# Kernel optimization log

Hardware: AMD Instinct MI355X
Metric: run time of the kernel (lower is better)

Reference implementation:

```python
import jax, jax.numpy as jnp
import numpy as np


def _sine_theta(v1, v2):
    # v1, v2: [..., 2] edge direction vectors
    cross = v1[..., 0] * v2[..., 1] - v1[..., 1] * v2[..., 0]
    k = jnp.linalg.norm(v1, axis=-1) * jnp.linalg.norm(v2, axis=-1)
    return cross / k


def setup_inputs() -> dict:
    key = jax.random.key(0)
    P, N = 16384, 1024  # P polygons, N points each (N % 4 == 0)
    x_list = jax.random.normal(key, (P, N, 2), dtype=jnp.float32)
    return {"x_list": x_list, "scale": 1}


def reference(x_list, scale):
    # x_list: [P, N, 2] stacked polygons (equivalent to the original python list
    # when all polygons have the same point count N).
    P, N, _ = x_list.shape
    segn = N // 4
    # close the polygon and form consecutive edge vectors v[k] = x[k+1] - x[k]
    xc = jnp.concatenate([x_list, x_list[:, :1]], axis=1)  # [P, N+1, 2]
    v = xc[:, 1:] - xc[:, :-1]                             # [P, N, 2]
    idx = jnp.arange(segn) * 3
    v1 = v[:, idx]       # edge i*3
    v2 = v[:, idx + 1]   # edge i*3+1
    v3 = v[:, idx + 2]   # edge i*3+2
    s12 = _sine_theta(v1, v2)   # [P, segn]
    sina = _sine_theta(v1, v3)  # [P, segn]
    direct = (s12 >= 0).astype(x_list.dtype)
    term = direct * jax.nn.relu(-sina) + (1.0 - direct) * jax.nn.relu(sina)
    seg_loss = term.sum(axis=1) / segn  # [P]
    return (seg_loss * scale).mean()
```

## Files before the change

### kernel.cpp

```cpp
#include <hip/hip_runtime.h>


#define N_PTS     1024
#define SEGN      (N_PTS / 4)
#define BLOCK     256
#define ROW_F4    385

__global__ __launch_bounds__(BLOCK)
void xing_partial_kernel(const float* __restrict__ x,
                         float*       __restrict__ partial)
{
    const int p = blockIdx.x;
    const int t = threadIdx.x;

    __shared__ float rowf[ROW_F4 * 4];

    const float4* src = reinterpret_cast<const float4*>(x + (size_t)p * (N_PTS * 2));
    float4* dst = reinterpret_cast<float4*>(rowf);
    dst[t] = src[t];
    if (t < ROW_F4 - BLOCK) dst[BLOCK + t] = src[BLOCK + t];
    __syncthreads();

    const float2* pts = reinterpret_cast<const float2*>(rowf);
    const float2 a = pts[3 * t + 0];
    const float2 b = pts[3 * t + 1];
    const float2 c = pts[3 * t + 2];
    const float2 d = pts[3 * t + 3];

    const float v1x = b.x - a.x, v1y = b.y - a.y;
    const float v2x = c.x - b.x, v2y = c.y - b.y;
    const float v3x = d.x - c.x, v3y = d.y - c.y;

    const float cross12 = v1x * v2y - v1y * v2x;
    const float cross13 = v1x * v3y - v1y * v3x;

    const float n1 = v1x * v1x + v1y * v1y;
    const float n3 = v3x * v3x + v3y * v3y;
    const float sina = cross13 * rsqrtf(n1 * n3);

    float term = (cross12 >= 0.0f) ? fmaxf(-sina, 0.0f) : fmaxf(sina, 0.0f);

    #pragma unroll
    for (int off = 32; off > 0; off >>= 1)
        term += __shfl_down(term, off, 64);

    __shared__ float wsum[BLOCK / 64];
    const int lane = t & 63;
    const int wid  = t >> 6;
    if (lane == 0) wsum[wid] = term;
    __syncthreads();

    if (t == 0) {
        partial[p] = (wsum[0] + wsum[1]) + (wsum[2] + wsum[3]);
    }
}

__global__ __launch_bounds__(BLOCK)
void xing_reduce_kernel(const float* __restrict__ partial,
                        const int*   __restrict__ scale_p,
                        float*       __restrict__ out,
                        int P)
{
    const int t = threadIdx.x;
    const float4* pf4 = reinterpret_cast<const float4*>(partial);
    const int nf4 = P / 4;

    float sum = 0.0f;
    for (int i = t; i < nf4; i += BLOCK) {
        float4 v = pf4[i];
        sum += (v.x + v.y) + (v.z + v.w);
    }

    #pragma unroll
    for (int off = 32; off > 0; off >>= 1)
        sum += __shfl_down(sum, off, 64);

    __shared__ float wsum[BLOCK / 64];
    const int lane = t & 63;
    const int wid  = t >> 6;
    if (lane == 0) wsum[wid] = sum;
    __syncthreads();

    if (t == 0) {
        const float total = (wsum[0] + wsum[1]) + (wsum[2] + wsum[3]);
        out[0] = total * (float)(*scale_p) / ((float)SEGN * (float)P);
    }
}

extern "C" void kernel_launch(void* const* d_in, const int* in_sizes, int n_in,
                              void* d_out, int out_size, void* d_ws, size_t ws_size,
                              hipStream_t stream)
{
    const float* x       = (const float*)d_in[0];
    const int*   scale_p = (const int*)d_in[1];
    float*       out     = (float*)d_out;
    float*       partial = (float*)d_ws;

    const int P = in_sizes[0] / (N_PTS * 2);

    xing_partial_kernel<<<P, BLOCK, 0, stream>>>(x, partial);
    xing_reduce_kernel<<<1, BLOCK, 0, stream>>>(partial, scale_p, out, P);
}
```

Measured before the change: 182.4 us.

## Process multiple polygons per block with register-prefetched double-buffered LDS

Each block now handles 8 polygons instead of one, so the grid is 8x smaller and the partial array shrinks. The next row is prefetched into registers while the current row is processed from a double-buffered LDS tile, overlapping global loads with compute. The cost is a per-row __syncthreads and fewer blocks, which lowers the number of memory requests in flight per CU. The kernel reads only 1.5 of every 2 rows' worth of data and is bound by memory latency and bandwidth.

After: 186.5 us. 1.02x slower.

```diff
diff --git a/kernel.cpp b/kernel.cpp
--- a/kernel.cpp
+++ b/kernel.cpp
@@ -4,55 +4,76 @@
 #define N_PTS     1024
 #define SEGN      (N_PTS / 4)
 #define BLOCK     256
+#define RPB       8
 #define ROW_F4    385
+#define ROW_STRIDE_F4 (N_PTS * 2 / 4)
 
 __global__ __launch_bounds__(BLOCK)
 void xing_partial_kernel(const float* __restrict__ x,
                          float*       __restrict__ partial)
 {
-    const int p = blockIdx.x;
     const int t = threadIdx.x;
+    const bool has2 = (t < ROW_F4 - BLOCK);
 
-    __shared__ float rowf[ROW_F4 * 4];
+    __shared__ float4 buf[2][ROW_F4];
 
-    const float4* src = reinterpret_cast<const float4*>(x + (size_t)p * (N_PTS * 2));
-    float4* dst = reinterpret_cast<float4*>(rowf);
-    dst[t] = src[t];
-    if (t < ROW_F4 - BLOCK) dst[BLOCK + t] = src[BLOCK + t];
+    const float4* src = reinterpret_cast<const float4*>(x)
+                      + (size_t)blockIdx.x * RPB * ROW_STRIDE_F4;
+
+    buf[0][t] = src[t];
+    if (has2) buf[0][BLOCK + t] = src[BLOCK + t];
     __syncthreads();
 
-    const float2* pts = reinterpret_cast<const float2*>(rowf);
-    const float2 a = pts[3 * t + 0];
-    const float2 b = pts[3 * t + 1];
-    const float2 c = pts[3 * t + 2];
-    const float2 d = pts[3 * t + 3];
+    float acc = 0.0f;
 
-    const float v1x = b.x - a.x, v1y = b.y - a.y;
-    const float v2x = c.x - b.x, v2y = c.y - b.y;
-    const float v3x = d.x - c.x, v3y = d.y - c.y;
+    #pragma unroll
+    for (int r = 0; r < RPB; ++r) {
+        float4 n0, n1;
+        if (r + 1 < RPB) {
+            const float4* nsrc = src + (size_t)(r + 1) * ROW_STRIDE_F4;
+            n0 = nsrc[t];
+            if (has2) n1 = nsrc[BLOCK + t];
+        }
 
-    const float cross12 = v1x * v2y - v1y * v2x;
-    const float cross13 = v1x * v3y - v1y * v3x;
+        const float2* pts = reinterpret_cast<const float2*>(buf[r & 1]);
+        const float2 a = pts[3 * t + 0];
+        const float2 b = pts[3 * t + 1];
+        const float2 c = pts[3 * t + 2];
+        const float2 d = pts[3 * t + 3];
 
-    const float n1 = v1x * v1x + v1y * v1y;
-    const float n3 = v3x * v3x + v3y * v3y;
-    const float sina = cross13 * rsqrtf(n1 * n3);
+        const float v1x = b.x - a.x, v1y = b.y - a.y;
+        const float v2x = c.x - b.x, v2y = c.y - b.y;
+        const float v3x = d.x - c.x, v3y = d.y - c.y;
 
-    float term = (cross12 >= 0.0f) ? fmaxf(-sina, 0.0f) : fmaxf(sina, 0.0f);
+        const float cross12 = v1x * v2y - v1y * v2x;
+        const float cross13 = v1x * v3y - v1y * v3x;
+
+        const float n1sq = v1x * v1x + v1y * v1y;
+        const float n3sq = v3x * v3x + v3y * v3y;
+        const float sina = cross13 * rsqrtf(n1sq * n3sq);
+
+        acc += (cross12 >= 0.0f) ? fmaxf(-sina, 0.0f) : fmaxf(sina, 0.0f);
+
+        if (r + 1 < RPB) {
+            float4* dst = buf[(r + 1) & 1];
+            dst[t] = n0;
+            if (has2) dst[BLOCK + t] = n1;
+        }
+        __syncthreads();
+    }
 
     #pragma unroll
     for (int off = 32; off > 0; off >>= 1)
-        term += __shfl_down(term, off, 64);
+        acc += __shfl_down(acc, off, 64);
 
     __shared__ float wsum[BLOCK / 64];
     const int lane = t & 63;
     const int wid  = t >> 6;
-    if (lane == 0) wsum[wid] = term;
+    if (lane == 0) wsum[wid] = acc;
     __syncthreads();
 
-    if (t == 0) {
-        partial[p] = (wsum[0] + wsum[1]) + (wsum[2] + wsum[3]);
-    }
+    if (t == 0)
+        partial[blockIdx.x] = (wsum[0] + wsum[1]) + (wsum[2] + wsum[3]);
 }
 
 __global__ __launch_bounds__(BLOCK)
@@ -62,10 +83,11 @@
                         int P)
 {
     const int t = threadIdx.x;
+    const int nf4 = (P / RPB) / 4;
     const float4* pf4 = reinterpret_cast<const float4*>(partial);
-    const int nf4 = P / 4;
 
     float sum = 0.0f;
+    #pragma unroll
     for (int i = t; i < nf4; i += BLOCK) {
         float4 v = pf4[i];
         sum += (v.x + v.y) + (v.z + v.w);
@@ -98,6 +120,6 @@
 
     const int P = in_sizes[0] / (N_PTS * 2);
 
-    xing_partial_kernel<<<P, BLOCK, 0, stream>>>(x, partial);
+    xing_partial_kernel<<<P / RPB, BLOCK, 0, stream>>>(x, partial);
     xing_reduce_kernel<<<1, BLOCK, 0, stream>>>(partial, scale_p, out, P);
 }
```
